# Optimization experiments

Measured on AMD Instinct MI355X. Metric: run time of the kernel, lower is better.

Reference implementation:

```python
import jax, jax.numpy as jnp
import numpy as np

D_MODEL = 1024
N_HEADS = 16
D_FF = 4096
EPS = 1e-5


def setup_inputs() -> dict:
    key = jax.random.key(0)
    ks = jax.random.split(key, 16)
    s = 0.02
    d, f = D_MODEL, D_FF
    return {
        "x": jax.random.normal(ks[0], (4, 2048, d), dtype=jnp.float32),
        "WQ": jax.random.normal(ks[1], (d, d), dtype=jnp.float32) * s,
        "bQ": jnp.zeros((d,), dtype=jnp.float32),
        "WK": jax.random.normal(ks[2], (d, d), dtype=jnp.float32) * s,
        "bK": jnp.zeros((d,), dtype=jnp.float32),
        "WV": jax.random.normal(ks[3], (d, d), dtype=jnp.float32) * s,
        "bV": jnp.zeros((d,), dtype=jnp.float32),
        "WO": jax.random.normal(ks[4], (d, d), dtype=jnp.float32) * s,
        "bO": jnp.zeros((d,), dtype=jnp.float32),
        "W1": jax.random.normal(ks[5], (f, d), dtype=jnp.float32) * s,
        "b1": jnp.zeros((f,), dtype=jnp.float32),
        "W2": jax.random.normal(ks[6], (d, f), dtype=jnp.float32) * s,
        "b2": jnp.zeros((d,), dtype=jnp.float32),
        "g1": jnp.ones((d,), dtype=jnp.float32),
        "be1": jnp.zeros((d,), dtype=jnp.float32),
        "g2": jnp.ones((d,), dtype=jnp.float32),
        "be2": jnp.zeros((d,), dtype=jnp.float32),
    }


def _layernorm(x, g, b):
    mu = jnp.mean(x, axis=-1, keepdims=True)
    var = jnp.mean(jnp.square(x - mu), axis=-1, keepdims=True)
    return (x - mu) * jax.lax.rsqrt(var + EPS) * g + b


def reference(x, WQ, bQ, WK, bK, WV, bV, WO, bO, W1, b1, W2, b2, g1, be1, g2, be2):
    B, T, D = x.shape
    H, dk = N_HEADS, D // N_HEADS
    # projections (torch Linear: x @ W.T + b), reshape to [B,H,T,dk]
    q = (x @ WQ.T + bQ).reshape(B, T, H, dk).transpose(0, 2, 1, 3)
    k = (x @ WK.T + bK).reshape(B, T, H, dk).transpose(0, 2, 1, 3)
    v = (x @ WV.T + bV).reshape(B, T, H, dk).transpose(0, 2, 1, 3)
    scores = jnp.einsum("bhqd,bhkd->bhqk", q, k) / jnp.sqrt(jnp.float32(dk))
    causal = jnp.tril(jnp.ones((T, T), dtype=bool))
    scores = jnp.where(causal[None, None], scores, jnp.float32(-jnp.inf))
    attn = jax.nn.softmax(scores, axis=-1)
    out = jnp.einsum("bhqk,bhkd->bhqd", attn, v)
    out = out.transpose(0, 2, 1, 3).reshape(B, T, D)
    attn_out = out @ WO.T + bO
    x = _layernorm(x + attn_out, g1, be1)
    ff = jax.nn.relu(x @ W1.T + b1) @ W2.T + b2
    return _layernorm(x + ff, g2, be2)
```

## Files before the change

kernel.cpp:

```cpp
#include <hip/hip_runtime.h>

typedef unsigned short u16;
typedef unsigned int u32;
typedef __bf16 bf16x8 __attribute__((ext_vector_type(8)));
typedef float f32x4 __attribute__((ext_vector_type(4)));
typedef float f32x16 __attribute__((ext_vector_type(16)));

__device__ __forceinline__ u16 f2bf(float f) {
  u32 u = __builtin_bit_cast(u32, f);
  u = (u + 0x7fffu + ((u >> 16) & 1u)) >> 16;
  return (u16)u;
}
__device__ __forceinline__ float bf2f(u16 h) {
  return __builtin_bit_cast(float, ((u32)h) << 16);
}

__device__ __forceinline__ void gll16(const u16* g, u16* l) {
  __builtin_amdgcn_global_load_lds((const __attribute__((address_space(1))) void*)g,
                                   (__attribute__((address_space(3))) void*)l, 16, 0, 0);
}

__device__ __forceinline__ void barrier() {
  asm volatile("" ::: "memory");
  __builtin_amdgcn_s_barrier();
  asm volatile("" ::: "memory");
}
__device__ __forceinline__ void waitv8() { asm volatile("s_waitcnt vmcnt(8)" ::: "memory"); }
__device__ __forceinline__ void waitv0() { asm volatile("s_waitcnt vmcnt(0)" ::: "memory"); }

__global__ __launch_bounds__(256) void cvt_all(const float* __restrict__ x,
                                               const float* __restrict__ WQ,
                                               const float* __restrict__ WK,
                                               const float* __restrict__ WV,
                                               const float* __restrict__ WO,
                                               const float* __restrict__ W1,
                                               const float* __restrict__ W2,
                                               u16* __restrict__ xb,
                                               u16* __restrict__ wqkvb,
                                               u16* __restrict__ wob,
                                               u16* __restrict__ w1b,
                                               u16* __restrict__ w2b) {
  const int S = 1 << 20;
  int i = (blockIdx.x * 256 + threadIdx.x) * 4;
  const float* src;
  u16* dst;
  if (i < 8 * S) { src = x + i; dst = xb + i; }
  else {
    int j = i - 8 * S;
    if (j < 3 * S)      { src = (j < S) ? WQ + j : (j < 2 * S) ? WK + (j - S) : WV + (j - 2 * S);
                          dst = wqkvb + j; }
    else if (j < 4 * S) { src = WO + (j - 3 * S); dst = wob + (j - 3 * S); }
    else if (j < 8 * S) { src = W1 + (j - 4 * S); dst = w1b + (j - 4 * S); }
    else                { src = W2 + (j - 8 * S); dst = w2b + (j - 8 * S); }
  }
  float4 v = *(const float4*)src;
  uint2 o;
  o.x = (u32)f2bf(v.x) | ((u32)f2bf(v.y) << 16);
  o.y = (u32)f2bf(v.z) | ((u32)f2bf(v.w) << 16);
  *(uint2*)dst = o;
}

template <int RELU, int QKV, int SPLIT>
__global__ __launch_bounds__(512, 2) void gemm256(const u16* __restrict__ A,
                                                  const u16* __restrict__ W,
                                                  const float* __restrict__ bias0,
                                                  void* __restrict__ C0,
                                                  int M, int N, int K,
                                                  const float* __restrict__ bias1,
                                                  void* __restrict__ C1,
                                                  const float* __restrict__ bias2,
                                                  void* __restrict__ C2,
                                                  int NBN) {
  __shared__ alignas(16) u16 lds[4 * 16384];
  const int tid = threadIdx.x;
  const int id = blockIdx.x;
  const int xcd = id & 7, r = id >> 3;
  int bm, bn, kz = 0, koff = 0, KL = K;
  if (SPLIT) {
    bn = (r & 3) << 8;
    const int q = r >> 2;
    bm = ((q & 3) * 8 + xcd) << 8;
    kz = q >> 2;
    KL = K >> 1;
    koff = kz * KL;
  } else {
    bn = (r % NBN) << 8;
    bm = ((r / NBN) * 8 + xcd) << 8;
  }
  const int wave = tid >> 6, lane = tid & 63;
  const int lr = lane & 15, quad = lane >> 4;
  const int wm = (wave >> 2) << 7;
  const int wn = (wave & 3) << 6;

  const int lrow = lane >> 2;
  const int lch = (lane & 3) ^ ((lane >> 3) & 3);
  const u16* Asrc = A + (size_t)(bm + wave * 16 + lrow) * K + koff + lch * 8;
  const u16* Wsrc = W + (size_t)(bn + wave * 16 + lrow) * K + koff + lch * 8;
  const size_t half = (size_t)128 * K;
  u16* dstbase = lds + wave * 512;

  const int NT = KL >> 5;
  const int fro = (quad ^ ((lr >> 1) & 3)) * 8;
  f32x4 acc[8][4] = {};

  #pragma unroll
  for (int t = 0; t < 3; t++) {
    u16* d = dstbase + t * 16384;
    gll16(Asrc + (size_t)t * 32, d);
    gll16(Asrc + (size_t)t * 32 + half, d + 4096);
    gll16(Wsrc + (size_t)t * 32, d + 8192);
    gll16(Wsrc + (size_t)t * 32 + half, d + 12288);
  }
  waitv8();
  barrier();

  for (int t = 0; t < NT; t++) {
    const u16* sa = lds + (t & 3) * 16384;
    const u16* sb = sa + 8192;
    const int tp = (t + 3 < NT) ? t + 3 : NT - 1;
    u16* d = dstbase + ((t + 3) & 3) * 16384;
    const size_t ko = (size_t)tp * 32;

    bf16x8 af[4], bfr[4];
    #pragma unroll
    for (int mi = 0; mi < 4; mi++)
      af[mi] = *(const bf16x8*)(sa + (wm + mi * 16 + lr) * 32 + fro);
    #pragma unroll
    for (int ni = 0; ni < 4; ni++)
      bfr[ni] = *(const bf16x8*)(sb + (wn + ni * 16 + lr) * 32 + fro);
    gll16(Asrc + ko, d);
    gll16(Asrc + ko + half, d + 4096);
    barrier();
    asm volatile("s_waitcnt lgkmcnt(0)" ::: "memory");
    __builtin_amdgcn_s_setprio(1);
    #pragma unroll
    for (int mi = 0; mi < 4; mi++)
      #pragma unroll
      for (int ni = 0; ni < 4; ni++)
        acc[mi][ni] = __builtin_amdgcn_mfma_f32_16x16x32_bf16(af[mi], bfr[ni], acc[mi][ni], 0, 0, 0);
    __builtin_amdgcn_s_setprio(0);
    barrier();

    #pragma unroll
    for (int mi = 0; mi < 4; mi++)
      af[mi] = *(const bf16x8*)(sa + (wm + 64 + mi * 16 + lr) * 32 + fro);
    gll16(Wsrc + ko, d + 8192);
    gll16(Wsrc + ko + half, d + 12288);
    barrier();
    asm volatile("s_waitcnt lgkmcnt(0)" ::: "memory");
    __builtin_amdgcn_s_setprio(1);
    #pragma unroll
    for (int mi = 0; mi < 4; mi++)
      #pragma unroll
      for (int ni = 0; ni < 4; ni++)
        acc[4 + mi][ni] = __builtin_amdgcn_mfma_f32_16x16x32_bf16(af[mi], bfr[ni], acc[4 + mi][ni], 0, 0, 0);
    __builtin_amdgcn_s_setprio(0);
    waitv8();
    barrier();
  }
  waitv0();

  const float* bp = bias0;
  void* outp = C0;
  float scale = 1.0f;
  int cb = bn, Nout = N, seg = 0;
  if (QKV) {
    Nout = 1024;
    seg = bn >> 10;
    cb = bn & 1023;
    if (seg == 0) scale = 0.125f * 1.44269504089f;
    else if (seg == 1) { bp = bias1; outp = C1; }
    else { bp = bias2; outp = C2; }
  }
  if (SPLIT && kz) outp = C1;

  if (QKV && seg == 2) {
    #pragma unroll
    for (int ni = 0; ni < 4; ni++) {
      const int col = cb + wn + ni * 16 + lr;
      const int hh = col >> 6, dl = col & 63;
      const float bv = bp[col];
      #pragma unroll
      for (int mi = 0; mi < 8; mi++) {
        const int row0 = bm + wm + mi * 16 + quad * 4;
        const int bb = row0 >> 11, tt = row0 & 2047;
        u16 pk[4];
        #pragma unroll
        for (int rg = 0; rg < 4; rg++) pk[rg] = f2bf(acc[mi][ni][rg] + bv);
        uint2 val;
        val.x = (u32)pk[0] | ((u32)pk[1] << 16);
        val.y = (u32)pk[2] | ((u32)pk[3] << 16);
        *(uint2*)(((u16*)outp) + ((size_t)((bb * 16 + hh) * 64 + dl)) * 2048 + tt) = val;
      }
    }
    return;
  }

  #pragma unroll
  for (int ni = 0; ni < 4; ni++) {
    const int col = cb + wn + ni * 16 + lr;
    const float bv = (SPLIT && kz) ? 0.0f : bp[col];
    #pragma unroll
    for (int mi = 0; mi < 8; mi++) {
      #pragma unroll
      for (int rg = 0; rg < 4; rg++) {
        int row = bm + wm + mi * 16 + quad * 4 + rg;
        float v = (acc[mi][ni][rg] + bv) * scale;
        if (RELU) v = fmaxf(v, 0.0f);
        ((u16*)outp)[(size_t)row * Nout + col] = f2bf(v);
      }
    }
  }
}

__global__ __launch_bounds__(256) void attn_mfma(const u16* __restrict__ qb,
                                                 const u16* __restrict__ kb,
                                                 const u16* __restrict__ vt,
                                                 u16* __restrict__ ctxb, int T) {
  __shared__ alignas(16) u16 shm[4 * 4096];
  const int tid = threadIdx.x;
  const int i = blockIdx.x;
  const int g = i & 63;
  const int p = 31 - (i >> 6);
  const int h = g >> 2, b = g & 3;
  const size_t base = ((size_t)(b * T)) * 1024 + h * 64;
  const size_t vbase = ((size_t)((b * 16 + h) * 64)) * T;
  const int lane = tid & 63, wave = tid >> 6;
  const int l31 = lane & 31, hh = lane >> 5;
  const int sub = wave & 1;
  const int kh = wave >> 1;
  const int srow = lane >> 3;
  const int sch = ((lane & 7) ^ srow) * 8;
  const int fs8 = l31 & 7;
  const int q0w = p * 64 + sub * 32;

  bf16x8 qf[4];
  #pragma unroll
  for (int ds = 0; ds < 4; ds++) {
    uint4 uq = *(const uint4*)(qb + base + (size_t)(q0w + l31) * 1024 + ds * 16 + hh * 8);
    qf[ds] = __builtin_bit_cast(bf16x8, uq);
  }
  f32x16 o0 = {}, o1 = {};
  float rsum = 0.0f;

  const int NI = (p >> 1) + 1;
  for (int j = 0; j < NI; j++) {
    const int ke = 2 * j;
    const int ko = (2 * j + 1 <= p) ? 2 * j + 1 : p;
    barrier();
    #pragma unroll
    for (int jj = 0; jj < 2; jj++) {
      const int rb = wave * 16 + jj * 8;
      const int rr = rb + srow;
      gll16(kb + base + (size_t)(ke * 64 + rr) * 1024 + sch, shm + rb * 64);
      gll16(kb + base + (size_t)(ko * 64 + rr) * 1024 + sch, shm + 4096 + rb * 64);
      gll16(vt + vbase + (size_t)rr * T + (size_t)(ke * 64) + sch, shm + 8192 + rb * 64);
      gll16(vt + vbase + (size_t)rr * T + (size_t)(ko * 64) + sch, shm + 12288 + rb * 64);
    }
    waitv0();
    barrier();
    const int kt = 2 * j + kh;
    if (kt <= p) {
      const u16* sKc = shm + kh * 4096;
      const u16* sVc = shm + 8192 + kh * 4096;

      f32x16 s0v = {}, s1v = {};
      #pragma unroll
      for (int ds = 0; ds < 4; ds++) {
        const int co = ((2 * ds + hh) ^ fs8) * 8;
        bf16x8 kf0 = *(const bf16x8*)(sKc + l31 * 64 + co);
        bf16x8 kf1 = *(const bf16x8*)(sKc + (32 + l31) * 64 + co);
        s0v = __builtin_amdgcn_mfma_f32_32x32x16_bf16(kf0, qf[ds], s0v, 0, 0, 0);
        s1v = __builtin_amdgcn_mfma_f32_32x32x16_bf16(kf1, qf[ds], s1v, 0, 0, 0);
      }

      if (kt == p) {
        const int qloc = (sub << 5) + l31;
        #pragma unroll
        for (int rg = 0; rg < 16; rg++) {
          const int key = (rg & 3) + 8 * (rg >> 2) + 4 * hh;
          if (key > qloc) s0v[rg] = -1e30f;
          if (key + 32 > qloc) s1v[rg] = -1e30f;
        }
      }

      float e[32];
      #pragma unroll
      for (int rg = 0; rg < 16; rg++) {
        e[rg] = __builtin_amdgcn_exp2f(s0v[rg]);
        e[16 + rg] = __builtin_amdgcn_exp2f(s1v[rg]);
        rsum += e[rg] + e[16 + rg];
      }

      union PW { u32 w[4]; bf16x8 v; } pf[4];
      #pragma unroll
      for (int t = 0; t < 2; t++) {
        #pragma unroll
        for (int sl = 0; sl < 2; sl++) {
          const int rb = t * 16 + sl * 8;
          u32 wa = __builtin_amdgcn_perm(__builtin_bit_cast(u32, e[rb + 1]), __builtin_bit_cast(u32, e[rb + 0]), 0x07060302u);
          u32 wb = __builtin_amdgcn_perm(__builtin_bit_cast(u32, e[rb + 5]), __builtin_bit_cast(u32, e[rb + 4]), 0x07060302u);
          u32 wc = __builtin_amdgcn_perm(__builtin_bit_cast(u32, e[rb + 3]), __builtin_bit_cast(u32, e[rb + 2]), 0x07060302u);
          u32 wd = __builtin_amdgcn_perm(__builtin_bit_cast(u32, e[rb + 7]), __builtin_bit_cast(u32, e[rb + 6]), 0x07060302u);
          asm("v_permlane32_swap_b32 %0, %1" : "+v"(wa), "+v"(wb));
          asm("v_permlane32_swap_b32 %0, %1" : "+v"(wc), "+v"(wd));
          pf[t * 2 + sl].w[0] = wa; pf[t * 2 + sl].w[1] = wc;
          pf[t * 2 + sl].w[2] = wb; pf[t * 2 + sl].w[3] = wd;
        }
      }

      #pragma unroll
      for (int s = 0; s < 4; s++) {
        const int co = ((2 * s + hh) ^ fs8) * 8;
        bf16x8 vf0 = *(const bf16x8*)(sVc + l31 * 64 + co);
        bf16x8 vf1 = *(const bf16x8*)(sVc + (32 + l31) * 64 + co);
        o0 = __builtin_amdgcn_mfma_f32_32x32x16_bf16(pf[s].v, vf0, o0, 0, 0, 0);
        o1 = __builtin_amdgcn_mfma_f32_32x32x16_bf16(pf[s].v, vf1, o1, 0, 0, 0);
      }
    }
  }

  rsum += __shfl_xor(rsum, 32);
  barrier();
  float* red = (float*)shm;
  if (kh == 1) {
    #pragma unroll
    for (int rg = 0; rg < 16; rg++) {
      red[sub * 2112 + rg * 64 + lane] = o0[rg];
      red[sub * 2112 + (16 + rg) * 64 + lane] = o1[rg];
    }
    red[sub * 2112 + 2048 + lane] = rsum;
  }
  barrier();
  if (kh == 0) {
    #pragma unroll
    for (int rg = 0; rg < 16; rg++) {
      o0[rg] += red[sub * 2112 + rg * 64 + lane];
      o1[rg] += red[sub * 2112 + (16 + rg) * 64 + lane];
    }
    rsum += red[sub * 2112 + 2048 + lane];
    float inv = 1.0f / rsum;
    #pragma unroll
    for (int rg = 0; rg < 16; rg++) {
      const int qr = (rg & 3) + 8 * (rg >> 2) + 4 * hh;
      float iv = __shfl(inv, qr);
      const size_t rowoff = base + (size_t)(q0w + qr) * 1024;
      ctxb[rowoff + l31] = f2bf(o0[rg] * iv);
      ctxb[rowoff + 32 + l31] = f2bf(o1[rg] * iv);
    }
  }
}

template <int ABF>
__global__ __launch_bounds__(256) void ln_kernel(const void* __restrict__ a,
                                                 const u16* __restrict__ b,
                                                 const u16* __restrict__ c,
                                                 const float* __restrict__ g,
                                                 const float* __restrict__ be,
                                                 float* __restrict__ of32,
                                                 u16* __restrict__ obf) {
  const int row = blockIdx.x;
  const int tid = threadIdx.x;
  const size_t base = (size_t)row * 1024;
  const int cc = tid * 4;
  float a0, a1, a2, a3;
  if (ABF) {
    uint2 ua = *(const uint2*)((const u16*)a + base + cc);
    a0 = bf2f(ua.x & 0xffff); a1 = bf2f(ua.x >> 16);
    a2 = bf2f(ua.y & 0xffff); a3 = bf2f(ua.y >> 16);
  } else {
    float4 xa = *(const float4*)((const float*)a + base + cc);
    a0 = xa.x; a1 = xa.y; a2 = xa.z; a3 = xa.w;
  }
  uint2 ub = *(const uint2*)(b + base + cc);
  uint2 uc = *(const uint2*)(c + base + cc);
  float v0 = a0 + bf2f(ub.x & 0xffff) + bf2f(uc.x & 0xffff);
  float v1 = a1 + bf2f(ub.x >> 16)    + bf2f(uc.x >> 16);
  float v2 = a2 + bf2f(ub.y & 0xffff) + bf2f(uc.y & 0xffff);
  float v3 = a3 + bf2f(ub.y >> 16)    + bf2f(uc.y >> 16);
  float s1 = v0 + v1 + v2 + v3;
  float s2 = v0 * v0 + v1 * v1 + v2 * v2 + v3 * v3;
  for (int off = 1; off < 64; off <<= 1) {
    s1 += __shfl_xor(s1, off);
    s2 += __shfl_xor(s2, off);
  }
  __shared__ float red[8];
  int wv = tid >> 6;
  if ((tid & 63) == 0) { red[wv] = s1; red[4 + wv] = s2; }
  __syncthreads();
  s1 = red[0] + red[1] + red[2] + red[3];
  s2 = red[4] + red[5] + red[6] + red[7];
  float mu = s1 * (1.0f / 1024.0f);
  float var = s2 * (1.0f / 1024.0f) - mu * mu;
  float rs = rsqrtf(var + 1e-5f);
  float4 gv = *(const float4*)(g + cc);
  float4 bev = *(const float4*)(be + cc);
  float y0 = (v0 - mu) * rs * gv.x + bev.x;
  float y1 = (v1 - mu) * rs * gv.y + bev.y;
  float y2 = (v2 - mu) * rs * gv.z + bev.z;
  float y3 = (v3 - mu) * rs * gv.w + bev.w;
  if (of32) {
    float4 o = make_float4(y0, y1, y2, y3);
    *(float4*)(of32 + base + cc) = o;
  }
  if (obf) {
    uint2 o;
    o.x = (u32)f2bf(y0) | ((u32)f2bf(y1) << 16);
    o.y = (u32)f2bf(y2) | ((u32)f2bf(y3) << 16);
    *(uint2*)(obf + base + cc) = o;
  }
}

extern "C" void kernel_launch(void* const* d_in, const int* in_sizes, int n_in,
                              void* d_out, int out_size, void* d_ws, size_t ws_size,
                              hipStream_t stream) {
  const int Mtok = 8192, D = 1024, F = 4096, T = 2048;
  const float* x   = (const float*)d_in[0];
  const float* WQ  = (const float*)d_in[1];
  const float* bQ  = (const float*)d_in[2];
  const float* WK  = (const float*)d_in[3];
  const float* bK  = (const float*)d_in[4];
  const float* WV  = (const float*)d_in[5];
  const float* bV  = (const float*)d_in[6];
  const float* WO  = (const float*)d_in[7];
  const float* bO  = (const float*)d_in[8];
  const float* W1  = (const float*)d_in[9];
  const float* b1  = (const float*)d_in[10];
  const float* W2  = (const float*)d_in[11];
  const float* b2  = (const float*)d_in[12];
  const float* g1  = (const float*)d_in[13];
  const float* be1 = (const float*)d_in[14];
  const float* g2  = (const float*)d_in[15];
  const float* be2 = (const float*)d_in[16];

  char* ws = (char*)d_ws;
  const size_t MB = 1024 * 1024;
  u16*  xb     = (u16*)(ws + 0);
  u16*  wqkvb  = (u16*)(ws + 16 * MB);
  u16*  wob    = (u16*)(ws + 22 * MB);
  u16*  w1b    = (u16*)(ws + 24 * MB);
  u16*  w2b    = (u16*)(ws + 32 * MB);
  u16*  qb     = (u16*)(ws + 40 * MB);
  u16*  kb     = (u16*)(ws + 56 * MB);
  u16*  vtb    = (u16*)(ws + 72 * MB);
  u16*  ctxb   = (u16*)(ws + 88 * MB);
  u16*  wp0    = (u16*)(ws + 104 * MB);
  u16*  wp1    = (u16*)(ws + 120 * MB);
  u16*  h1b    = (u16*)(ws + 136 * MB);
  u16*  ff1b   = (u16*)(ws + 40 * MB);
  u16*  fp0    = (u16*)(ws + 0);
  u16*  fp1    = (u16*)(ws + 16 * MB);
  float* out   = (float*)d_out;

  dim3 blk(256);
  dim3 blk512(512);
  cvt_all<<<(20 << 20) / 1024, blk, 0, stream>>>(x, WQ, WK, WV, WO, W1, W2,
                                                 xb, wqkvb, wob, w1b, w2b);

  gemm256<0, 1, 0><<<dim3(384), blk512, 0, stream>>>(xb, wqkvb, bQ, qb, Mtok, 3072, D,
                                                     bK, kb, bV, vtb, 12);
  attn_mfma<<<dim3(2048), blk, 0, stream>>>(qb, kb, vtb, ctxb, T);

  gemm256<0, 0, 1><<<dim3(256), blk512, 0, stream>>>(ctxb, wob, bO, wp0, Mtok, D, D,
                                                     nullptr, wp1, nullptr, nullptr, 4);
  ln_kernel<0><<<Mtok, blk, 0, stream>>>(x, wp0, wp1, g1, be1, nullptr, h1b);

  gemm256<1, 0, 0><<<dim3(512), blk512, 0, stream>>>(h1b, w1b, b1, ff1b, Mtok, F, D,
                                                     nullptr, nullptr, nullptr, nullptr, 16);
  gemm256<0, 0, 1><<<dim3(256), blk512, 0, stream>>>(ff1b, w2b, b2, fp0, Mtok, D, F,
                                                     nullptr, fp1, nullptr, nullptr, 4);
  ln_kernel<1><<<Mtok, blk, 0, stream>>>(h1b, fp0, fp1, g2, be2, out, (u16*)nullptr);
}
```

Before: 489.0 us.

## Shrink GEMM tiles to 256x128 with double-buffered LDS and higher occupancy

Changes the GEMM block tile from 256x256 to 256x128, giving each wave a 64x64 sub-tile. The 4-stage LDS pipeline becomes a simpler 2-stage double buffer, and the launch bound rises to 4 blocks per CU. Grids double so more blocks cover the CUs. The aim is better occupancy and more blocks in flight for latency hiding. The cost is lower arithmetic intensity per block and less prefetch depth.

```diff
diff --git a/kernel.cpp b/kernel.cpp
--- a/kernel.cpp
+++ b/kernel.cpp
@@ -25,7 +25,7 @@
   __builtin_amdgcn_s_barrier();
   asm volatile("" ::: "memory");
 }
-__device__ __forceinline__ void waitv8() { asm volatile("s_waitcnt vmcnt(8)" ::: "memory"); }
+__device__ __forceinline__ void waitv3() { asm volatile("s_waitcnt vmcnt(3)" ::: "memory"); }
 __device__ __forceinline__ void waitv0() { asm volatile("s_waitcnt vmcnt(0)" ::: "memory"); }
 
 __global__ __launch_bounds__(256) void cvt_all(const float* __restrict__ x,
@@ -61,7 +61,7 @@
 }
 
 template <int RELU, int QKV, int SPLIT>
-__global__ __launch_bounds__(512, 2) void gemm256(const u16* __restrict__ A,
+__global__ __launch_bounds__(512, 4) void gemm256(const u16* __restrict__ A,
                                                   const u16* __restrict__ W,
                                                   const float* __restrict__ bias0,
                                                   void* __restrict__ C0,
@@ -71,56 +71,53 @@
                                                   const float* __restrict__ bias2,
                                                   void* __restrict__ C2,
                                                   int NBN) {
-  __shared__ alignas(16) u16 lds[4 * 16384];
+  __shared__ alignas(16) u16 lds[2 * 12288];
   const int tid = threadIdx.x;
   const int id = blockIdx.x;
   const int xcd = id & 7, r = id >> 3;
   int bm, bn, kz = 0, koff = 0, KL = K;
   if (SPLIT) {
-    bn = (r & 3) << 8;
-    const int q = r >> 2;
+    bn = (r & 7) << 7;
+    const int q = r >> 3;
     bm = ((q & 3) * 8 + xcd) << 8;
     kz = q >> 2;
     KL = K >> 1;
     koff = kz * KL;
   } else {
-    bn = (r % NBN) << 8;
+    bn = (r % NBN) << 7;
     bm = ((r / NBN) * 8 + xcd) << 8;
   }
   const int wave = tid >> 6, lane = tid & 63;
   const int lr = lane & 15, quad = lane >> 4;
-  const int wm = (wave >> 2) << 7;
-  const int wn = (wave & 3) << 6;
+  const int wm = (wave >> 1) << 6;
+  const int wn = (wave & 1) << 6;
 
   const int lrow = lane >> 2;
   const int lch = (lane & 3) ^ ((lane >> 3) & 3);
-  const u16* Asrc = A + (size_t)(bm + wave * 16 + lrow) * K + koff + lch * 8;
+  const u16* Asrc = A + (size_t)(bm + wave * 32 + lrow) * K + koff + lch * 8;
   const u16* Wsrc = W + (size_t)(bn + wave * 16 + lrow) * K + koff + lch * 8;
-  const size_t half = (size_t)128 * K;
-  u16* dstbase = lds + wave * 512;
+  const size_t rK16 = (size_t)16 * K;
 
   const int NT = KL >> 5;
   const int fro = (quad ^ ((lr >> 1) & 3)) * 8;
-  f32x4 acc[8][4] = {};
-
-  #pragma unroll
-  for (int t = 0; t < 3; t++) {
-    u16* d = dstbase + t * 16384;
-    gll16(Asrc + (size_t)t * 32, d);
-    gll16(Asrc + (size_t)t * 32 + half, d + 4096);
-    gll16(Wsrc + (size_t)t * 32, d + 8192);
-    gll16(Wsrc + (size_t)t * 32 + half, d + 12288);
-  }
-  waitv8();
-  barrier();
+  f32x4 acc[4][4] = {};
+
+#define STAGE(tt) { const int tp_ = ((tt) < NT) ? (tt) : NT - 1;    \
+    const size_t ko_ = (size_t)tp_ * 32;                                                            \
+    u16* b_ = lds + ((tt) & 1) * 12288;                                                             \
+    gll16(Asrc + ko_, b_ + wave * 1024);                                                            \
+    gll16(Asrc + ko_ + rK16, b_ + wave * 1024 + 512);                                               \
+    gll16(Wsrc + ko_, b_ + 8192 + wave * 512); }
+
+  STAGE(0);
 
   for (int t = 0; t < NT; t++) {
-    const u16* sa = lds + (t & 3) * 16384;
+    barrier();
+    STAGE(t + 1);
+    waitv3();
+    barrier();
+    const u16* sa = lds + (t & 1) * 12288;
     const u16* sb = sa + 8192;
-    const int tp = (t + 3 < NT) ? t + 3 : NT - 1;
-    u16* d = dstbase + ((t + 3) & 3) * 16384;
-    const size_t ko = (size_t)tp * 32;
-
     bf16x8 af[4], bfr[4];
     #pragma unroll
     for (int mi = 0; mi < 4; mi++)
@@ -128,9 +125,6 @@
     #pragma unroll
     for (int ni = 0; ni < 4; ni++)
       bfr[ni] = *(const bf16x8*)(sb + (wn + ni * 16 + lr) * 32 + fro);
-    gll16(Asrc + ko, d);
-    gll16(Asrc + ko + half, d + 4096);
-    barrier();
     asm volatile("s_waitcnt lgkmcnt(0)" ::: "memory");
     __builtin_amdgcn_s_setprio(1);
     #pragma unroll
@@ -139,26 +133,9 @@
       for (int ni = 0; ni < 4; ni++)
         acc[mi][ni] = __builtin_amdgcn_mfma_f32_16x16x32_bf16(af[mi], bfr[ni], acc[mi][ni], 0, 0, 0);
     __builtin_amdgcn_s_setprio(0);
-    barrier();
-
-    #pragma unroll
-    for (int mi = 0; mi < 4; mi++)
-      af[mi] = *(const bf16x8*)(sa + (wm + 64 + mi * 16 + lr) * 32 + fro);
-    gll16(Wsrc + ko, d + 8192);
-    gll16(Wsrc + ko + half, d + 12288);
-    barrier();
-    asm volatile("s_waitcnt lgkmcnt(0)" ::: "memory");
-    __builtin_amdgcn_s_setprio(1);
-    #pragma unroll
-    for (int mi = 0; mi < 4; mi++)
-      #pragma unroll
-      for (int ni = 0; ni < 4; ni++)
-        acc[4 + mi][ni] = __builtin_amdgcn_mfma_f32_16x16x32_bf16(af[mi], bfr[ni], acc[4 + mi][ni], 0, 0, 0);
-    __builtin_amdgcn_s_setprio(0);
-    waitv8();
-    barrier();
   }
   waitv0();
+#undef STAGE
 
   const float* bp = bias0;
   void* outp = C0;
@@ -181,7 +158,7 @@
       const int hh = col >> 6, dl = col & 63;
       const float bv = bp[col];
       #pragma unroll
-      for (int mi = 0; mi < 8; mi++) {
+      for (int mi = 0; mi < 4; mi++) {
         const int row0 = bm + wm + mi * 16 + quad * 4;
         const int bb = row0 >> 11, tt = row0 & 2047;
         u16 pk[4];
@@ -201,7 +178,7 @@
     const int col = cb + wn + ni * 16 + lr;
     const float bv = (SPLIT && kz) ? 0.0f : bp[col];
     #pragma unroll
-    for (int mi = 0; mi < 8; mi++) {
+    for (int mi = 0; mi < 4; mi++) {
       #pragma unroll
       for (int rg = 0; rg < 4; rg++) {
         int row = bm + wm + mi * 16 + quad * 4 + rg;
@@ -457,17 +434,17 @@
   cvt_all<<<(20 << 20) / 1024, blk, 0, stream>>>(x, WQ, WK, WV, WO, W1, W2,
                                                  xb, wqkvb, wob, w1b, w2b);
 
-  gemm256<0, 1, 0><<<dim3(384), blk512, 0, stream>>>(xb, wqkvb, bQ, qb, Mtok, 3072, D,
-                                                     bK, kb, bV, vtb, 12);
+  gemm256<0, 1, 0><<<dim3(768), blk512, 0, stream>>>(xb, wqkvb, bQ, qb, Mtok, 3072, D,
+                                                     bK, kb, bV, vtb, 24);
   attn_mfma<<<dim3(2048), blk, 0, stream>>>(qb, kb, vtb, ctxb, T);
 
-  gemm256<0, 0, 1><<<dim3(256), blk512, 0, stream>>>(ctxb, wob, bO, wp0, Mtok, D, D,
-                                                     nullptr, wp1, nullptr, nullptr, 4);
+  gemm256<0, 0, 1><<<dim3(512), blk512, 0, stream>>>(ctxb, wob, bO, wp0, Mtok, D, D,
+                                                     nullptr, wp1, nullptr, nullptr, 8);
   ln_kernel<0><<<Mtok, blk, 0, stream>>>(x, wp0, wp1, g1, be1, nullptr, h1b);
 
-  gemm256<1, 0, 0><<<dim3(512), blk512, 0, stream>>>(h1b, w1b, b1, ff1b, Mtok, F, D,
-                                                     nullptr, nullptr, nullptr, nullptr, 16);
-  gemm256<0, 0, 1><<<dim3(256), blk512, 0, stream>>>(ff1b, w2b, b2, fp0, Mtok, D, F,
-                                                     nullptr, fp1, nullptr, nullptr, 4);
+  gemm256<1, 0, 0><<<dim3(1024), blk512, 0, stream>>>(h1b, w1b, b1, ff1b, Mtok, F, D,
+                                                      nullptr, nullptr, nullptr, nullptr, 32);
+  gemm256<0, 0, 1><<<dim3(512), blk512, 0, stream>>>(ff1b, w2b, b2, fp0, Mtok, D, F,
+                                                     nullptr, fp1, nullptr, nullptr, 8);
   ln_kernel<1><<<Mtok, blk, 0, stream>>>(h1b, fp0, fp1, g2, be2, out, (u16*)nullptr);
 }
```

Result: faster. 455.1 us (-6.9%).
